# Performance work log

Measured on AMD Instinct MI355X. Metric: run time of the kernel, lower is better.

The kernel has to match this reference:

```python
import jax, jax.numpy as jnp
import numpy as np

H, DH = 16, 64  # heads, dim_head; inner = H*DH = 1024
EPS = 1e-5


def _ln(t, g, b):
    mu = jnp.mean(t, axis=-1, keepdims=True)
    var = jnp.var(t, axis=-1, keepdims=True)
    return (t - mu) * jax.lax.rsqrt(var + EPS) * g + b


def _split_heads(t):
    b, n, _ = t.shape
    return t.reshape(b, n, H, DH).transpose(0, 2, 1, 3)  # (b,h,n,dh)


def setup_inputs() -> dict:
    key = jax.random.key(0)
    ks = jax.random.split(key, 5)
    B, S, M, D = 16, 64, 4096, 1024  # S must equal DH (see source einsum quirk)
    return {
        "x": jax.random.normal(ks[0], (B, S, D), jnp.float32),
        "latents": jax.random.normal(ks[1], (B, M, D), jnp.float32),
        "ln_x_g": jnp.ones((D,), jnp.float32),
        "ln_x_b": jnp.zeros((D,), jnp.float32),
        "ln_l_g": jnp.ones((D,), jnp.float32),
        "ln_l_b": jnp.zeros((D,), jnp.float32),
        "Wq": jax.random.normal(ks[2], (D, H * DH), jnp.float32) * 0.02,
        "Wkv": jax.random.normal(ks[3], (D, 2 * H * DH), jnp.float32) * 0.02,
        "Wout": jax.random.normal(ks[4], (H * DH, D), jnp.float32) * 0.02,
    }


def reference(x, latents, ln_x_g, ln_x_b, ln_l_g, ln_l_b, Wq, Wkv, Wout):
    scale = DH ** -0.5
    xn = _ln(x, ln_x_g, ln_x_b)          # (B,S,D)
    ln = _ln(latents, ln_l_g, ln_l_b)    # (B,M,D)
    q = _split_heads(ln @ Wq) * scale    # (B,H,M,DH)
    k, v = map(_split_heads, jnp.split(xn @ Wkv, 2, axis=-1))  # (B,H,S,DH)
    sim = jnp.einsum('bhid,bhjd->bhij', q, k)                  # (B,H,M,S)
    sim = sim - jax.lax.stop_gradient(jnp.max(sim, axis=-1, keepdims=True))
    attn = jax.nn.softmax(sim, axis=-1)
    # Faithful to source: einsum('b h i d, b h j d -> b h i j', attn, v)
    # contracts attn's S dim with v's DH dim (requires S == DH); out = attn @ v^T.
    out = jnp.einsum('bhis,bhjs->bhij', attn, v)               # (B,H,M,S)
    b, _, m, _ = out.shape
    out = out.transpose(0, 2, 1, 3).reshape(b, m, H * DH)      # (B,M,inner)
    return out @ Wout                                          # (B,M,D)
```

## Files before the change

### kernel.cpp

```cpp
#include <hip/hip_runtime.h>
#include <stdint.h>

#define B_ 16
#define S_ 64
#define M_ 4096
#define D_ 1024
#define H_ 16
#define DH_ 64

typedef unsigned short ushort_t;
typedef __attribute__((ext_vector_type(8))) __bf16 bfrag;
typedef __attribute__((ext_vector_type(4))) float f32x4;

__device__ __forceinline__ ushort_t f2bf(float f) {
  union { float f; uint32_t u; } v; v.f = f;
  uint32_t r = v.u + 0x7fffu + ((v.u >> 16) & 1u);
  return (ushort_t)(r >> 16);
}

__device__ __forceinline__ void gload_lds16(const void* g, void* l) {
  __builtin_amdgcn_global_load_lds((const __attribute__((address_space(1))) void*)g,
                                   (__attribute__((address_space(3))) void*)l, 16, 0, 0);
}

__device__ __forceinline__ f32x4 mfma16x16x32(bfrag a, bfrag b, f32x4 c) {
  return __builtin_amdgcn_mfma_f32_16x16x32_bf16(a, b, c, 0, 0, 0);
}

__device__ __forceinline__ int fsw(int r) { return (((r >> 2) & 3) << 1) | (r & 1); }

__global__ __launch_bounds__(256) void ln_rows_kernel(
    const float* __restrict__ x, const float* __restrict__ g,
    const float* __restrict__ bta, ushort_t* __restrict__ out) {
  const int row = blockIdx.x;
  const int t = threadIdx.x;
  const float4* xr = (const float4*)(x + (size_t)row * D_);
  float4 v = xr[t];
  float s = v.x + v.y + v.z + v.w;
  float ss = v.x * v.x + v.y * v.y + v.z * v.z + v.w * v.w;
#pragma unroll
  for (int o = 32; o >= 1; o >>= 1) { s += __shfl_down(s, o); ss += __shfl_down(ss, o); }
  __shared__ float red[16];
  const int wid = t >> 6;
  if ((t & 63) == 0) { red[wid] = s; red[8 + wid] = ss; }
  __syncthreads();
  float tot = red[0] + red[1] + red[2] + red[3];
  float tot2 = red[8] + red[9] + red[10] + red[11];
  float mu = tot * (1.0f / D_);
  float var = tot2 * (1.0f / D_) - mu * mu;
  float rstd = rsqrtf(var + 1e-5f);
  float4 gg = ((const float4*)g)[t];
  float4 bb = ((const float4*)bta)[t];
  ushort_t ob[4];
  ob[0] = f2bf((v.x - mu) * rstd * gg.x + bb.x);
  ob[1] = f2bf((v.y - mu) * rstd * gg.y + bb.y);
  ob[2] = f2bf((v.z - mu) * rstd * gg.z + bb.z);
  ob[3] = f2bf((v.w - mu) * rstd * gg.w + bb.w);
  *(uint2*)(out + (size_t)row * D_ + t * 4) = *(const uint2*)ob;
}

__global__ void transpose_cast_kernel(const float* __restrict__ W, ushort_t* __restrict__ WT,
                                      int N, float scale) {
  __shared__ float tile[32][33];
  const int n0 = blockIdx.x * 32, k0 = blockIdx.y * 32;
  const int tx = threadIdx.x, ty = threadIdx.y;
#pragma unroll
  for (int i = ty; i < 32; i += 8)
    tile[i][tx] = W[(size_t)(k0 + i) * N + n0 + tx];
  __syncthreads();
#pragma unroll
  for (int i = ty; i < 32; i += 8)
    WT[(size_t)(n0 + i) * D_ + k0 + tx] = f2bf(tile[tx][i] * scale);
}

__global__ __launch_bounds__(256) void gemm_kv_kernel(
    const ushort_t* __restrict__ A, const ushort_t* __restrict__ Bt,
    ushort_t* __restrict__ kb, ushort_t* __restrict__ vb) {
  __shared__ __align__(16) ushort_t sA[128 * 32];
  __shared__ __align__(16) ushort_t sB[128 * 32];
  const int tid = threadIdx.x, wid = tid >> 6, lane = tid & 63;
  const size_t arow0 = (size_t)blockIdx.x * 128;
  const size_t brow0 = (size_t)blockIdx.y * 128;
  const int wr = (wid >> 1) * 64, wc = (wid & 1) * 64;
  const int srow = tid >> 2, scol = (tid & 3) * 8;
  const ushort_t* ga = A + (arow0 + srow) * (size_t)D_ + scol;
  const ushort_t* gb = Bt + (brow0 + srow) * (size_t)D_ + scol;
  const int frow = lane & 15, kslot = (lane >> 4) * 8;
  f32x4 acc[4][4] = {};
  for (int k0 = 0; k0 < D_; k0 += 32) {
    gload_lds16(ga, sA + wid * 512);
    gload_lds16(ga + 64 * (size_t)D_, sA + 2048 + wid * 512);
    gload_lds16(gb, sB + wid * 512);
    gload_lds16(gb + 64 * (size_t)D_, sB + 2048 + wid * 512);
    ga += 32; gb += 32;
    __syncthreads();
    bfrag af[4], bfv[4];
#pragma unroll
    for (int m = 0; m < 4; ++m)
      af[m] = *(const bfrag*)&sA[(wr + m * 16 + frow) * 32 + kslot];
#pragma unroll
    for (int n = 0; n < 4; ++n)
      bfv[n] = *(const bfrag*)&sB[(wc + n * 16 + frow) * 32 + kslot];
#pragma unroll
    for (int m = 0; m < 4; ++m)
#pragma unroll
      for (int n = 0; n < 4; ++n)
        acc[m][n] = mfma16x16x32(af[m], bfv[n], acc[m][n]);
    __syncthreads();
  }
  const int erow = (lane >> 4) * 4, ecol = lane & 15;
#pragma unroll
  for (int m = 0; m < 4; ++m)
#pragma unroll
    for (int n = 0; n < 4; ++n)
#pragma unroll
      for (int r = 0; r < 4; ++r) {
        size_t i = arow0 + wr + m * 16 + erow + r;
        int bb = (int)(i >> 6), s = (int)(i & 63);
        size_t n2 = brow0 + wc + n * 16 + ecol;
        ushort_t val = f2bf(acc[m][n][r]);
        ushort_t* dst = (n2 < 1024) ? kb : vb;
        size_t hh = (n2 & 1023) >> 6, d = n2 & 63;
        dst[(((size_t)bb * H_ + hh) * S_ + s) * DH_ + d] = val;
      }
}

template <int MODE>
__global__ __launch_bounds__(256, 3) void gemm97_kernel(
    const ushort_t* __restrict__ A, const ushort_t* __restrict__ Bt,
    const ushort_t* __restrict__ kbuf, const ushort_t* __restrict__ vbuf,
    void* __restrict__ Cout) {
  __shared__ __align__(16) ushort_t lds[24576];
  ushort_t* const sA = lds;
  ushort_t* const sB = lds + 4096;
  const int tid = threadIdx.x, wid = tid >> 6, lane = tid & 63;
  const int frow = lane & 15, klo = lane >> 4;
  const int wr = (wid >> 1) * 64, wc = (wid & 1) * 64;

  const int l = ((int)blockIdx.x & 7) * 512 + ((int)blockIdx.x >> 3);
  const int mblk = l >> 3, nblk = l & 7;
  const size_t arow0 = (size_t)mblk * 128;
  const size_t bcol0 = (size_t)nblk * 128;

  const int r0 = tid >> 2;
  const int gsrc = (tid & 3) ^ ((tid >> 3) & 3);
  const ushort_t* gA = A + (arow0 + r0) * (size_t)D_ + gsrc * 8;
  const ushort_t* gB = Bt + (bcol0 + r0) * (size_t)D_ + gsrc * 8;
  const int rasw = (klo ^ ((frow >> 1) & 3)) * 8;

  f32x4 acc[4][4] = {};
  for (int k0 = 0; k0 < 32; ++k0) {
    gload_lds16(gA, sA + wid * 512);
    gload_lds16(gA + 64 * (size_t)D_, sA + 2048 + wid * 512);
    gload_lds16(gB, sB + wid * 512);
    gload_lds16(gB + 64 * (size_t)D_, sB + 2048 + wid * 512);
    gA += 32; gB += 32;
    __syncthreads();
    bfrag a_[4], b_[4];
#pragma unroll
    for (int mf = 0; mf < 4; ++mf)
      a_[mf] = *(const bfrag*)&sA[(wr + mf * 16 + frow) * 32 + rasw];
#pragma unroll
    for (int nf = 0; nf < 4; ++nf)
      b_[nf] = *(const bfrag*)&sB[(wc + nf * 16 + frow) * 32 + rasw];
#pragma unroll
    for (int mf = 0; mf < 4; ++mf)
#pragma unroll
      for (int nf = 0; nf < 4; ++nf)
        acc[mf][nf] = mfma16x16x32(a_[mf], b_[nf], acc[mf][nf]);
    __syncthreads();
  }

  if constexpr (MODE == 0) {
    float* C = (float*)Cout;
#pragma unroll
    for (int m = 0; m < 4; ++m)
#pragma unroll
      for (int n = 0; n < 4; ++n)
#pragma unroll
        for (int r = 0; r < 4; ++r)
          C[(arow0 + wr + m * 16 + klo * 4 + r) * 1024 + bcol0 + wc + n * 16 + frow] =
              acc[m][n][r];
  } else {
    ushort_t* W = &lds[8192 + wid * 4096];
    ushort_t* out1 = (ushort_t*)Cout;
    const int head = nblk * 2 + (wid & 1);
    const int bbatch = mblk >> 5;
    const size_t kvbase = ((size_t)bbatch * H_ + head) * (size_t)(S_ * DH_);

#pragma unroll
    for (int m2 = 0; m2 < 4; ++m2)
#pragma unroll
      for (int r = 0; r < 4; ++r) {
        const int row = m2 * 16 + klo * 4 + r;
        const int fs = fsw(row);
#pragma unroll
        for (int n = 0; n < 4; ++n) {
          const int cc = n * 16 + frow;
          W[row * 64 + ((((cc >> 3) ^ fs) << 3) | (cc & 7))] = f2bf(acc[m2][n][r]);
        }
      }
    bfrag kb[4][2];
#pragma unroll
    for (int nf = 0; nf < 4; ++nf)
#pragma unroll
      for (int kk = 0; kk < 2; ++kk)
        kb[nf][kk] = *(const bfrag*)&kbuf[kvbase + (nf * 16 + frow) * 64 + kk * 32 + klo * 8];
    f32x4 s[4][4] = {};
#pragma unroll
    for (int m2 = 0; m2 < 4; ++m2) {
      const int row = m2 * 16 + frow;
      const int fs = fsw(row);
#pragma unroll
      for (int kk = 0; kk < 2; ++kk) {
        bfrag qa = *(const bfrag*)&W[row * 64 + (((kk * 4 + klo) ^ fs) << 3)];
#pragma unroll
        for (int nf = 0; nf < 4; ++nf)
          s[m2][nf] = mfma16x16x32(qa, kb[nf][kk], s[m2][nf]);
      }
    }
#pragma unroll
    for (int m2 = 0; m2 < 4; ++m2)
#pragma unroll
      for (int r = 0; r < 4; ++r) {
        float a0 = s[m2][0][r], a1 = s[m2][1][r], a2 = s[m2][2][r], a3 = s[m2][3][r];
        float mx = fmaxf(fmaxf(a0, a1), fmaxf(a2, a3));
#pragma unroll
        for (int o = 1; o < 16; o <<= 1) mx = fmaxf(mx, __shfl_xor(mx, o));
        a0 = __expf(a0 - mx); a1 = __expf(a1 - mx);
        a2 = __expf(a2 - mx); a3 = __expf(a3 - mx);
        float sm = (a0 + a1) + (a2 + a3);
#pragma unroll
        for (int o = 1; o < 16; o <<= 1) sm += __shfl_xor(sm, o);
        const float inv = 1.0f / sm;
        s[m2][0][r] = a0 * inv; s[m2][1][r] = a1 * inv;
        s[m2][2][r] = a2 * inv; s[m2][3][r] = a3 * inv;
      }
#pragma unroll
    for (int m2 = 0; m2 < 4; ++m2)
#pragma unroll
      for (int r = 0; r < 4; ++r) {
        const int row = m2 * 16 + klo * 4 + r;
        const int fs = fsw(row);
#pragma unroll
        for (int n = 0; n < 4; ++n) {
          const int cc = n * 16 + frow;
          W[row * 64 + ((((cc >> 3) ^ fs) << 3) | (cc & 7))] = f2bf(s[m2][n][r]);
        }
      }
    bfrag vb[4][2];
#pragma unroll
    for (int nf = 0; nf < 4; ++nf)
#pragma unroll
      for (int kk = 0; kk < 2; ++kk)
        vb[nf][kk] = *(const bfrag*)&vbuf[kvbase + (nf * 16 + frow) * 64 + kk * 32 + klo * 8];
    f32x4 o[4][4] = {};
#pragma unroll
    for (int m2 = 0; m2 < 4; ++m2) {
      const int row = m2 * 16 + frow;
      const int fs = fsw(row);
#pragma unroll
      for (int kk = 0; kk < 2; ++kk) {
        bfrag pa = *(const bfrag*)&W[row * 64 + (((kk * 4 + klo) ^ fs) << 3)];
#pragma unroll
        for (int nf = 0; nf < 4; ++nf)
          o[m2][nf] = mfma16x16x32(pa, vb[nf][kk], o[m2][nf]);
      }
    }
#pragma unroll
    for (int m2 = 0; m2 < 4; ++m2)
#pragma unroll
      for (int r = 0; r < 4; ++r) {
        const int row = m2 * 16 + klo * 4 + r;
        const int fs = fsw(row);
#pragma unroll
        for (int n = 0; n < 4; ++n) {
          const int cc = n * 16 + frow;
          W[row * 64 + ((((cc >> 3) ^ fs) << 3) | (cc & 7))] = f2bf(o[m2][n][r]);
        }
      }
    const size_t grow0 = arow0 + wr;
#pragma unroll
    for (int it = 0; it < 8; ++it) {
      const int idx = it * 64 + lane;
      const int rr = idx >> 3, gs = idx & 7;
      const int gcol = (gs ^ fsw(rr)) << 3;
      *(uint4*)&out1[(grow0 + rr) * 1024 + head * 64 + gcol] =
          *(const uint4*)&W[rr * 64 + gs * 8];
    }
  }
}

extern "C" void kernel_launch(void* const* d_in, const int* in_sizes, int n_in,
                              void* d_out, int out_size, void* d_ws, size_t ws_size,
                              hipStream_t stream) {
  const float* x = (const float*)d_in[0];
  const float* lat = (const float*)d_in[1];
  const float* lxg = (const float*)d_in[2];
  const float* lxb = (const float*)d_in[3];
  const float* llg = (const float*)d_in[4];
  const float* llb = (const float*)d_in[5];
  const float* Wq = (const float*)d_in[6];
  const float* Wkv = (const float*)d_in[7];
  const float* Wout = (const float*)d_in[8];
  float* out = (float*)d_out;
  char* ws = (char*)d_ws;

  ushort_t* xn = (ushort_t*)(ws);
  ushort_t* wqT = (ushort_t*)(ws + (2ull << 20));
  ushort_t* wkvT = (ushort_t*)(ws + (4ull << 20));
  ushort_t* woT = (ushort_t*)(ws + (8ull << 20));
  ushort_t* kbuf = (ushort_t*)(ws + (10ull << 20));
  ushort_t* vbuf = (ushort_t*)(ws + (12ull << 20));
  ushort_t* out1 = (ushort_t*)(ws + (14ull << 20));
  ushort_t* lnl = (ushort_t*)d_out;

  dim3 tb(32, 8);
  transpose_cast_kernel<<<dim3(1024 / 32, 32), tb, 0, stream>>>(Wq, wqT, 1024, 0.125f);
  transpose_cast_kernel<<<dim3(2048 / 32, 32), tb, 0, stream>>>(Wkv, wkvT, 2048, 1.0f);
  transpose_cast_kernel<<<dim3(1024 / 32, 32), tb, 0, stream>>>(Wout, woT, 1024, 1.0f);
  ln_rows_kernel<<<B_ * S_, 256, 0, stream>>>(x, lxg, lxb, xn);
  ln_rows_kernel<<<B_ * M_, 256, 0, stream>>>(lat, llg, llb, lnl);
  gemm_kv_kernel<<<dim3(8, 16), 256, 0, stream>>>(xn, wkvT, kbuf, vbuf);
  gemm97_kernel<1><<<4096, 256, 0, stream>>>(lnl, wqT, kbuf, vbuf, out1);
  gemm97_kernel<0><<<4096, 256, 0, stream>>>(out1, woT, nullptr, nullptr, out);
}
```

Baseline: 549.9 us.

## Use 256x256 tiles with 32x32x16 MFMA and triple-buffered async LDS pipeline

Replaces the 128x128-tile GEMM with a 256x256 tile per block, where each wave computes 128x128 using 32x32x16 bf16 MFMAs. K-slices are loaded into a three-slot LDS ring with two stages in flight, so there is one barrier per iteration instead of two. The fused attention epilogue now loops over two row halves and two heads per wave. This raises arithmetic intensity and hides global latency, but it drops occupancy to one block per CU and uses many more accumulator registers.

```diff
diff --git a/kernel.cpp b/kernel.cpp
--- a/kernel.cpp
+++ b/kernel.cpp
@@ -11,6 +11,7 @@
 typedef unsigned short ushort_t;
 typedef __attribute__((ext_vector_type(8))) __bf16 bfrag;
 typedef __attribute__((ext_vector_type(4))) float f32x4;
+typedef __attribute__((ext_vector_type(16))) float f32x16;
 
 __device__ __forceinline__ ushort_t f2bf(float f) {
   union { float f; uint32_t u; } v; v.f = f;
@@ -23,11 +24,12 @@
                                    (__attribute__((address_space(3))) void*)l, 16, 0, 0);
 }
 
-__device__ __forceinline__ f32x4 mfma16x16x32(bfrag a, bfrag b, f32x4 c) {
+__device__ __forceinline__ f32x4 mfma16(bfrag a, bfrag b, f32x4 c) {
   return __builtin_amdgcn_mfma_f32_16x16x32_bf16(a, b, c, 0, 0, 0);
 }
-
-__device__ __forceinline__ int fsw(int r) { return (((r >> 2) & 3) << 1) | (r & 1); }
+__device__ __forceinline__ f32x16 mfma32(bfrag a, bfrag b, f32x16 c) {
+  return __builtin_amdgcn_mfma_f32_32x32x16_bf16(a, b, c, 0, 0, 0);
+}
 
 __global__ __launch_bounds__(256) void ln_rows_kernel(
     const float* __restrict__ x, const float* __restrict__ g,
@@ -105,7 +107,7 @@
     for (int m = 0; m < 4; ++m)
 #pragma unroll
       for (int n = 0; n < 4; ++n)
-        acc[m][n] = mfma16x16x32(af[m], bfv[n], acc[m][n]);
+        acc[m][n] = mfma16(af[m], bfv[n], acc[m][n]);
     __syncthreads();
   }
   const int erow = (lane >> 4) * 4, ecol = lane & 15;
@@ -126,168 +128,200 @@
 }
 
 template <int MODE>
-__global__ __launch_bounds__(256, 3) void gemm97_kernel(
+__global__ __launch_bounds__(256, 1) void gemm_fat_kernel(
     const ushort_t* __restrict__ A, const ushort_t* __restrict__ Bt,
     const ushort_t* __restrict__ kbuf, const ushort_t* __restrict__ vbuf,
     void* __restrict__ Cout) {
-  __shared__ __align__(16) ushort_t lds[24576];
-  ushort_t* const sA = lds;
-  ushort_t* const sB = lds + 4096;
+  __shared__ __align__(16) ushort_t lds[49152];
   const int tid = threadIdx.x, wid = tid >> 6, lane = tid & 63;
+  const int l31 = lane & 31, l5 = lane >> 5;
   const int frow = lane & 15, klo = lane >> 4;
-  const int wr = (wid >> 1) * 64, wc = (wid & 1) * 64;
-
-  const int l = ((int)blockIdx.x & 7) * 512 + ((int)blockIdx.x >> 3);
-  const int mblk = l >> 3, nblk = l & 7;
-  const size_t arow0 = (size_t)mblk * 128;
-  const size_t bcol0 = (size_t)nblk * 128;
+  const int wm = wid >> 1, wn = wid & 1;
+
+  const int l = ((int)blockIdx.x & 7) * 128 + ((int)blockIdx.x >> 3);
+  const int mblk = l >> 2, nblk = l & 3;
+  const size_t arow0 = (size_t)mblk * 256;
+  const size_t bcol0 = (size_t)nblk * 256;
 
   const int r0 = tid >> 2;
   const int gsrc = (tid & 3) ^ ((tid >> 3) & 3);
-  const ushort_t* gA = A + (arow0 + r0) * (size_t)D_ + gsrc * 8;
-  const ushort_t* gB = Bt + (bcol0 + r0) * (size_t)D_ + gsrc * 8;
-  const int rasw = (klo ^ ((frow >> 1) & 3)) * 8;
-
-  f32x4 acc[4][4] = {};
-  for (int k0 = 0; k0 < 32; ++k0) {
-    gload_lds16(gA, sA + wid * 512);
-    gload_lds16(gA + 64 * (size_t)D_, sA + 2048 + wid * 512);
-    gload_lds16(gB, sB + wid * 512);
-    gload_lds16(gB + 64 * (size_t)D_, sB + 2048 + wid * 512);
-    gA += 32; gB += 32;
-    __syncthreads();
-    bfrag a_[4], b_[4];
-#pragma unroll
-    for (int mf = 0; mf < 4; ++mf)
-      a_[mf] = *(const bfrag*)&sA[(wr + mf * 16 + frow) * 32 + rasw];
-#pragma unroll
-    for (int nf = 0; nf < 4; ++nf)
-      b_[nf] = *(const bfrag*)&sB[(wc + nf * 16 + frow) * 32 + rasw];
-#pragma unroll
-    for (int mf = 0; mf < 4; ++mf)
+  const ushort_t* pA = A + (arow0 + r0) * (size_t)D_ + gsrc * 8;
+  const ushort_t* pB = Bt + (bcol0 + r0) * (size_t)D_ + gsrc * 8;
+
+#define STAGE(G, SLOT)                                                          \
+  do {                                                                          \
+    const size_t ko_ = (size_t)((G) < 32 ? (G) : 31) * 32;                      \
+    _Pragma("unroll") for (int j = 0; j < 4; ++j)                               \
+        gload_lds16(pA + (size_t)j * 64 * D_ + ko_,                             \
+                    &lds[(SLOT) * 16384 + j * 2048 + wid * 512]);               \
+    _Pragma("unroll") for (int j = 0; j < 4; ++j)                               \
+        gload_lds16(pB + (size_t)j * 64 * D_ + ko_,                             \
+                    &lds[(SLOT) * 16384 + 8192 + j * 2048 + wid * 512]);        \
+  } while (0)
+
+  STAGE(0, 0);
+  STAGE(1, 1);
+
+  const int sw3 = (l31 >> 1) & 3;
+  const int aBase = wm * 4096 + l31 * 32;
+  const int bBase = 8192 + wn * 4096 + l31 * 32;
+
+  f32x16 acc[4][4] = {};
+  int sl = 0;
+  for (int g = 0; g < 32; ++g) {
+    asm volatile("s_waitcnt vmcnt(8)" ::: "memory");
+    __builtin_amdgcn_s_barrier();
+    asm volatile("" ::: "memory");
+    const int snext = (sl + 2 >= 3) ? sl - 1 : sl + 2;
+    STAGE(g + 2, snext);
+    const int sb = sl * 16384;
+    bfrag af[4][2], bf[4][2];
+#pragma unroll
+    for (int kk = 0; kk < 2; ++kk) {
+      const int gk = (((kk << 1) | l5) ^ sw3) * 8;
+#pragma unroll
+      for (int mf = 0; mf < 4; ++mf)
+        af[mf][kk] = *(const bfrag*)&lds[sb + aBase + mf * 1024 + gk];
 #pragma unroll
       for (int nf = 0; nf < 4; ++nf)
-        acc[mf][nf] = mfma16x16x32(a_[mf], b_[nf], acc[mf][nf]);
-    __syncthreads();
+        bf[nf][kk] = *(const bfrag*)&lds[sb + bBase + nf * 1024 + gk];
+    }
+#pragma unroll
+    for (int kk = 0; kk < 2; ++kk)
+#pragma unroll
+      for (int mf = 0; mf < 4; ++mf)
+#pragma unroll
+        for (int nf = 0; nf < 4; ++nf)
+          acc[mf][nf] = mfma32(af[mf][kk], bf[nf][kk], acc[mf][nf]);
+    sl = (sl + 1 >= 3) ? 0 : sl + 1;
   }
+  asm volatile("s_waitcnt vmcnt(0)" ::: "memory");
+  __builtin_amdgcn_s_barrier();
+  asm volatile("" ::: "memory");
+#undef STAGE
 
   if constexpr (MODE == 0) {
     float* C = (float*)Cout;
 #pragma unroll
-    for (int m = 0; m < 4; ++m)
-#pragma unroll
-      for (int n = 0; n < 4; ++n)
-#pragma unroll
-        for (int r = 0; r < 4; ++r)
-          C[(arow0 + wr + m * 16 + klo * 4 + r) * 1024 + bcol0 + wc + n * 16 + frow] =
-              acc[m][n][r];
+    for (int m2 = 0; m2 < 4; ++m2)
+#pragma unroll
+      for (int n2 = 0; n2 < 4; ++n2)
+#pragma unroll
+        for (int r = 0; r < 16; ++r) {
+          const int row = m2 * 32 + (r & 3) + 8 * (r >> 2) + 4 * l5;
+          C[(arow0 + wm * 128 + row) * 1024 + bcol0 + wn * 128 + n2 * 32 + l31] =
+              acc[m2][n2][r];
+        }
   } else {
-    ushort_t* W = &lds[8192 + wid * 4096];
+    ushort_t* W = &lds[wid * 4096];
     ushort_t* out1 = (ushort_t*)Cout;
-    const int head = nblk * 2 + (wid & 1);
-    const int bbatch = mblk >> 5;
-    const size_t kvbase = ((size_t)bbatch * H_ + head) * (size_t)(S_ * DH_);
-
-#pragma unroll
-    for (int m2 = 0; m2 < 4; ++m2)
-#pragma unroll
-      for (int r = 0; r < 4; ++r) {
-        const int row = m2 * 16 + klo * 4 + r;
-        const int fs = fsw(row);
-#pragma unroll
-        for (int n = 0; n < 4; ++n) {
-          const int cc = n * 16 + frow;
-          W[row * 64 + ((((cc >> 3) ^ fs) << 3) | (cc & 7))] = f2bf(acc[m2][n][r]);
+    const int bbatch = mblk >> 4;
+#pragma unroll
+    for (int rh = 0; rh < 2; ++rh)
+#pragma unroll
+      for (int h2 = 0; h2 < 2; ++h2) {
+        const int head = nblk * 4 + wn * 2 + h2;
+        const size_t kvbase = ((size_t)bbatch * H_ + head) * (size_t)(S_ * DH_);
+#pragma unroll
+        for (int m2i = 0; m2i < 2; ++m2i)
+#pragma unroll
+          for (int n2i = 0; n2i < 2; ++n2i)
+#pragma unroll
+            for (int r = 0; r < 16; ++r) {
+              const int row = m2i * 32 + (r & 3) + 8 * (r >> 2) + 4 * l5;
+              const int col = n2i * 32 + l31;
+              W[row * 64 + ((((col >> 3) ^ (row & 7)) << 3) | (col & 7))] =
+                  f2bf(acc[rh * 2 + m2i][h2 * 2 + n2i][r]);
+            }
+        bfrag kb[4][2];
+#pragma unroll
+        for (int nf = 0; nf < 4; ++nf)
+#pragma unroll
+          for (int kk = 0; kk < 2; ++kk)
+            kb[nf][kk] = *(const bfrag*)&kbuf[kvbase + (nf * 16 + frow) * 64 +
+                                              kk * 32 + klo * 8];
+        f32x4 s[4][4] = {};
+#pragma unroll
+        for (int mm = 0; mm < 4; ++mm) {
+          const int row = mm * 16 + frow;
+#pragma unroll
+          for (int kk = 0; kk < 2; ++kk) {
+            bfrag qa = *(const bfrag*)&W[row * 64 + (((kk * 4 + klo) ^ (frow & 7)) << 3)];
+#pragma unroll
+            for (int nf = 0; nf < 4; ++nf)
+              s[mm][nf] = mfma16(qa, kb[nf][kk], s[mm][nf]);
+          }
+        }
+#pragma unroll
+        for (int mm = 0; mm < 4; ++mm)
+#pragma unroll
+          for (int r = 0; r < 4; ++r) {
+            float a0 = s[mm][0][r], a1 = s[mm][1][r], a2 = s[mm][2][r], a3 = s[mm][3][r];
+            float mx = fmaxf(fmaxf(a0, a1), fmaxf(a2, a3));
+#pragma unroll
+            for (int o = 1; o < 16; o <<= 1) mx = fmaxf(mx, __shfl_xor(mx, o));
+            a0 = __expf(a0 - mx); a1 = __expf(a1 - mx);
+            a2 = __expf(a2 - mx); a3 = __expf(a3 - mx);
+            float sm = (a0 + a1) + (a2 + a3);
+#pragma unroll
+            for (int o = 1; o < 16; o <<= 1) sm += __shfl_xor(sm, o);
+            const float inv = 1.0f / sm;
+            s[mm][0][r] = a0 * inv; s[mm][1][r] = a1 * inv;
+            s[mm][2][r] = a2 * inv; s[mm][3][r] = a3 * inv;
+          }
+#pragma unroll
+        for (int mm = 0; mm < 4; ++mm)
+#pragma unroll
+          for (int r = 0; r < 4; ++r) {
+            const int row = mm * 16 + klo * 4 + r;
+#pragma unroll
+            for (int nf = 0; nf < 4; ++nf) {
+              const int col = nf * 16 + frow;
+              W[row * 64 + ((((col >> 3) ^ (row & 7)) << 3) | (col & 7))] =
+                  f2bf(s[mm][nf][r]);
+            }
+          }
+        bfrag vb[4][2];
+#pragma unroll
+        for (int nf = 0; nf < 4; ++nf)
+#pragma unroll
+          for (int kk = 0; kk < 2; ++kk)
+            vb[nf][kk] = *(const bfrag*)&vbuf[kvbase + (nf * 16 + frow) * 64 +
+                                              kk * 32 + klo * 8];
+        f32x4 o[4][4] = {};
+#pragma unroll
+        for (int mm = 0; mm < 4; ++mm) {
+          const int row = mm * 16 + frow;
+#pragma unroll
+          for (int kk = 0; kk < 2; ++kk) {
+            bfrag pa = *(const bfrag*)&W[row * 64 + (((kk * 4 + klo) ^ (frow & 7)) << 3)];
+#pragma unroll
+            for (int nf = 0; nf < 4; ++nf)
+              o[mm][nf] = mfma16(pa, vb[nf][kk], o[mm][nf]);
+          }
+        }
+#pragma unroll
+        for (int mm = 0; mm < 4; ++mm)
+#pragma unroll
+          for (int r = 0; r < 4; ++r) {
+            const int row = mm * 16 + klo * 4 + r;
+#pragma unroll
+            for (int nf = 0; nf < 4; ++nf) {
+              const int col = nf * 16 + frow;
+              W[row * 64 + ((((col >> 3) ^ (row & 7)) << 3) | (col & 7))] =
+                  f2bf(o[mm][nf][r]);
+            }
+          }
+        const size_t grow0 = arow0 + wm * 128 + rh * 64;
+#pragma unroll
+        for (int it = 0; it < 8; ++it) {
+          const int idx = it * 64 + lane;
+          const int rr = idx >> 3, gs = idx & 7;
+          const int gcol = (gs ^ (rr & 7)) << 3;
+          *(uint4*)&out1[(grow0 + rr) * 1024 + head * 64 + gcol] =
+              *(const uint4*)&W[rr * 64 + gs * 8];
         }
       }
-    bfrag kb[4][2];
-#pragma unroll
-    for (int nf = 0; nf < 4; ++nf)
-#pragma unroll
-      for (int kk = 0; kk < 2; ++kk)
-        kb[nf][kk] = *(const bfrag*)&kbuf[kvbase + (nf * 16 + frow) * 64 + kk * 32 + klo * 8];
-    f32x4 s[4][4] = {};
-#pragma unroll
-    for (int m2 = 0; m2 < 4; ++m2) {
-      const int row = m2 * 16 + frow;
-      const int fs = fsw(row);
-#pragma unroll
-      for (int kk = 0; kk < 2; ++kk) {
-        bfrag qa = *(const bfrag*)&W[row * 64 + (((kk * 4 + klo) ^ fs) << 3)];
-#pragma unroll
-        for (int nf = 0; nf < 4; ++nf)
-          s[m2][nf] = mfma16x16x32(qa, kb[nf][kk], s[m2][nf]);
-      }
-    }
-#pragma unroll
-    for (int m2 = 0; m2 < 4; ++m2)
-#pragma unroll
-      for (int r = 0; r < 4; ++r) {
-        float a0 = s[m2][0][r], a1 = s[m2][1][r], a2 = s[m2][2][r], a3 = s[m2][3][r];
-        float mx = fmaxf(fmaxf(a0, a1), fmaxf(a2, a3));
-#pragma unroll
-        for (int o = 1; o < 16; o <<= 1) mx = fmaxf(mx, __shfl_xor(mx, o));
-        a0 = __expf(a0 - mx); a1 = __expf(a1 - mx);
-        a2 = __expf(a2 - mx); a3 = __expf(a3 - mx);
-        float sm = (a0 + a1) + (a2 + a3);
-#pragma unroll
-        for (int o = 1; o < 16; o <<= 1) sm += __shfl_xor(sm, o);
-        const float inv = 1.0f / sm;
-        s[m2][0][r] = a0 * inv; s[m2][1][r] = a1 * inv;
-        s[m2][2][r] = a2 * inv; s[m2][3][r] = a3 * inv;
-      }
-#pragma unroll
-    for (int m2 = 0; m2 < 4; ++m2)
-#pragma unroll
-      for (int r = 0; r < 4; ++r) {
-        const int row = m2 * 16 + klo * 4 + r;
-        const int fs = fsw(row);
-#pragma unroll
-        for (int n = 0; n < 4; ++n) {
-          const int cc = n * 16 + frow;
-          W[row * 64 + ((((cc >> 3) ^ fs) << 3) | (cc & 7))] = f2bf(s[m2][n][r]);
-        }
-      }
-    bfrag vb[4][2];
-#pragma unroll
-    for (int nf = 0; nf < 4; ++nf)
-#pragma unroll
-      for (int kk = 0; kk < 2; ++kk)
-        vb[nf][kk] = *(const bfrag*)&vbuf[kvbase + (nf * 16 + frow) * 64 + kk * 32 + klo * 8];
-    f32x4 o[4][4] = {};
-#pragma unroll
-    for (int m2 = 0; m2 < 4; ++m2) {
-      const int row = m2 * 16 + frow;
-      const int fs = fsw(row);
-#pragma unroll
-      for (int kk = 0; kk < 2; ++kk) {
-        bfrag pa = *(const bfrag*)&W[row * 64 + (((kk * 4 + klo) ^ fs) << 3)];
-#pragma unroll
-        for (int nf = 0; nf < 4; ++nf)
-          o[m2][nf] = mfma16x16x32(pa, vb[nf][kk], o[m2][nf]);
-      }
-    }
-#pragma unroll
-    for (int m2 = 0; m2 < 4; ++m2)
-#pragma unroll
-      for (int r = 0; r < 4; ++r) {
-        const int row = m2 * 16 + klo * 4 + r;
-        const int fs = fsw(row);
-#pragma unroll
-        for (int n = 0; n < 4; ++n) {
-          const int cc = n * 16 + frow;
-          W[row * 64 + ((((cc >> 3) ^ fs) << 3) | (cc & 7))] = f2bf(o[m2][n][r]);
-        }
-      }
-    const size_t grow0 = arow0 + wr;
-#pragma unroll
-    for (int it = 0; it < 8; ++it) {
-      const int idx = it * 64 + lane;
-      const int rr = idx >> 3, gs = idx & 7;
-      const int gcol = (gs ^ fsw(rr)) << 3;
-      *(uint4*)&out1[(grow0 + rr) * 1024 + head * 64 + gcol] =
-          *(const uint4*)&W[rr * 64 + gs * 8];
-    }
   }
 }
 
@@ -322,6 +356,6 @@
   ln_rows_kernel<<<B_ * S_, 256, 0, stream>>>(x, lxg, lxb, xn);
   ln_rows_kernel<<<B_ * M_, 256, 0, stream>>>(lat, llg, llb, lnl);
   gemm_kv_kernel<<<dim3(8, 16), 256, 0, stream>>>(xn, wkvT, kbuf, vbuf);
-  gemm97_kernel<1><<<4096, 256, 0, stream>>>(lnl, wqT, kbuf, vbuf, out1);
-  gemm97_kernel<0><<<4096, 256, 0, stream>>>(out1, woT, nullptr, nullptr, out);
-}
+  gemm_fat_kernel<1><<<1024, 256, 0, stream>>>(lnl, wqT, kbuf, vbuf, out1);
+  gemm_fat_kernel<0><<<1024, 256, 0, stream>>>(out1, woT, nullptr, nullptr, out);
+}
```

Result: slower. 584.7 us (+6.3%).
